# Kernel tuning notes

Measured on AMD Instinct MI355X. Metric: run time of the kernel, lower is better.

The kernel has to match this reference:

```python
import jax, jax.numpy as jnp
import numpy as np

SEQ_LEN = 32
B, H, E, HID = 2048, 512, 512, 16
BN_EPS = 1e-5

def _mlp(x, w1, b1, g, bt, m, v, w2, b2):
    # Linear -> BatchNorm1d(eval) -> ReLU -> Linear
    h = x @ w1 + b1
    h = (h - m) * jax.lax.rsqrt(v + BN_EPS) * g + bt
    h = jnp.maximum(h, 0.0)
    return h @ w2 + b2

def setup_inputs() -> dict:
    key = jax.random.key(0)
    ks = jax.random.split(key, 24)
    def rn(k, shp, s=0.05):
        return jax.random.normal(k, shp, dtype=jnp.float32) * s
    inp = {
        'last_pos': jax.random.uniform(ks[0], (B, 2), dtype=jnp.float32),
        'hh': rn(ks[1], (1, B, H), 1.0),
        'ch': rn(ks[2], (1, B, H), 1.0),
        'se_w1': rn(ks[3], (2, HID)),
        'se_b1': rn(ks[4], (HID,)),
        'se_g': jax.random.uniform(ks[5], (HID,), dtype=jnp.float32) + 0.5,
        'se_bt': rn(ks[6], (HID,)),
        'se_m': rn(ks[7], (HID,)),
        'se_v': jax.random.uniform(ks[8], (HID,), dtype=jnp.float32) + 0.5,
        'se_w2': rn(ks[9], (HID, E)),
        'se_b2': rn(ks[10], (E,)),
        'w_ih': rn(ks[11], (4 * H, E)),
        'w_hh': rn(ks[12], (4 * H, H)),
        'b_ih': rn(ks[13], (4 * H,)),
        'b_hh': rn(ks[14], (4 * H,)),
        'hp_w1': rn(ks[15], (H, HID)),
        'hp_b1': rn(ks[16], (HID,)),
        'hp_g': jax.random.uniform(ks[17], (HID,), dtype=jnp.float32) + 0.5,
        'hp_bt': rn(ks[18], (HID,)),
        'hp_m': rn(ks[19], (HID,)),
        'hp_v': jax.random.uniform(ks[20], (HID,), dtype=jnp.float32) + 0.5,
        'hp_w2': rn(ks[21], (HID, 2)),
        'hp_b2': rn(ks[22], (2,)),
    }
    return inp

def reference(last_pos, hh, ch, se_w1, se_b1, se_g, se_bt, se_m, se_v, se_w2, se_b2,
              w_ih, w_hh, b_ih, b_hh,
              hp_w1, hp_b1, hp_g, hp_bt, hp_m, hp_v, hp_w2, hp_b2):
    h0, c0 = hh[0], ch[0]  # num_layers == 1

    def step(carry, _):
        h, c, lp = carry
        x = _mlp(lp, se_w1, se_b1, se_g, se_bt, se_m, se_v, se_w2, se_b2)  # [B,E]
        gates = x @ w_ih.T + b_ih + h @ w_hh.T + b_hh                      # [B,4H]
        i, f, g, o = jnp.split(gates, 4, axis=-1)
        i = jax.nn.sigmoid(i)
        f = jax.nn.sigmoid(f)
        g = jnp.tanh(g)
        o = jax.nn.sigmoid(o)
        c = f * c + i * g
        h = o * jnp.tanh(c)
        pos_rel = _mlp(h, hp_w1, hp_b1, hp_g, hp_bt, hp_m, hp_v, hp_w2, hp_b2)  # [B,2]
        # relative_to_abs on a length-1 sequence == pos_rel + last_pos, then sigmoid
        lp = jax.nn.sigmoid(pos_rel + lp)
        return (h, c, lp), lp

    _, traj = jax.lax.scan(step, (h0, c0, last_pos), None, length=SEQ_LEN)
    return traj  # [seq_len, batch, 2]
```

## Files before the change

kernel.cpp:

```cpp
#include <hip/hip_runtime.h>


#define TSEQ  32
#define BATCH 2048
#define HDIM  512
#define GDIM  2048
#define NBLK  256
#define NTHR  512
#define DEPTH 8

typedef __bf16 bf16x8 __attribute__((ext_vector_type(8)));
typedef float  f32x16 __attribute__((ext_vector_type(16)));
typedef unsigned long long u64;

#define BS_OFF     0
#define HPW_OFF    131072
#define UNI_OFF    147456
#define H1_OFF     157696
#define LPS_OFF    161792
#define PRM_OFF    162816
#define LDS_TOTAL  163360

#define WS_W1F    0
#define WS_BIASF  131072
#define WS_FLAGS  139264
#define WS_HATOM  141312

__device__ __forceinline__ unsigned f2bf(float f) {
  unsigned u = __float_as_uint(f);
  u += 0x7fffu + ((u >> 16) & 1u);
  return u >> 16;
}
__device__ __forceinline__ float bf2f(unsigned short b) {
  return __uint_as_float(((unsigned)b) << 16);
}
__device__ __forceinline__ u64 ld8(const void* p) {
  return __hip_atomic_load((const u64*)p, __ATOMIC_RELAXED, __HIP_MEMORY_SCOPE_AGENT);
}
__device__ __forceinline__ void st8(void* p, u64 v) {
  __hip_atomic_store((u64*)p, v, __ATOMIC_RELAXED, __HIP_MEMORY_SCOPE_AGENT);
}
__device__ __forceinline__ unsigned ld4(const unsigned* p) {
  return __hip_atomic_load(p, __ATOMIC_RELAXED, __HIP_MEMORY_SCOPE_AGENT);
}
__device__ __forceinline__ void st4(unsigned* p, unsigned v) {
  __hip_atomic_store(p, v, __ATOMIC_RELAXED, __HIP_MEMORY_SCOPE_AGENT);
}
__device__ __forceinline__ void l2_inv() {
  asm volatile("buffer_inv sc1" ::: "memory");
}
#define QB(x, imm) __uint_as_float((unsigned)__builtin_amdgcn_mov_dpp((int)__float_as_uint(x), imm, 0xF, 0xF, true))

struct KParams {
  const float *last_pos, *ch0, *w_hh;
  const float *se_w1, *se_b1, *se_g, *se_bt, *se_m, *se_v;
  const float *hp_w1, *hp_b1, *hp_g, *hp_bt, *hp_m, *hp_v, *hp_w2, *hp_b2;
  const float *W1f_g, *bias_f;
  char* hatom;
  unsigned* flags;
  float* out;
};

__global__ __launch_bounds__(256) void decoder_setup(
    const float* __restrict__ w_ih, const float* __restrict__ se_w2,
    const float* __restrict__ se_b2, const float* __restrict__ b_ih,
    const float* __restrict__ b_hh, const float* __restrict__ hh,
    float* __restrict__ W1f_g, float* __restrict__ bias_f,
    char* __restrict__ hatom) {
  int bid = blockIdx.x, tid = threadIdx.x;
  if (bid < 256) {
    __shared__ float wrow[8 * 512];
    __shared__ float ps[256];
    __shared__ float psB[128];
    int r0 = bid * 8;
    #pragma unroll
    for (int i = 0; i < 4; ++i) {
      int idx = i * 256 + tid;
      ((float4*)wrow)[idx] = ((const float4*)(w_ih + (size_t)r0 * 512))[idx];
    }
    __syncthreads();
    {
      int r = tid >> 5, q = (tid >> 1) & 15, half = tid & 1;
      const float* sw = se_w2 + (size_t)q * 512 + half * 256;
      const float* wr = wrow + r * 512 + half * 256;
      float s = 0.f;
      #pragma unroll 8
      for (int e = 0; e < 256; ++e) s += sw[e] * wr[e];
      ps[tid] = s;
    }
    if (tid < 128) {
      int r = tid >> 4, seg = tid & 15;
      const float* wr = wrow + r * 512 + seg * 32;
      const float* sb = se_b2 + seg * 32;
      float s = 0.f;
      #pragma unroll
      for (int e = 0; e < 32; ++e) s += sb[e] * wr[e];
      psB[tid] = s;
    }
    __syncthreads();
    if (tid < 128) {
      int r = tid >> 4, q = tid & 15;
      W1f_g[(r0 + r) * 16 + q] = ps[r * 32 + q * 2] + ps[r * 32 + q * 2 + 1];
    } else if (tid < 136) {
      int r = tid - 128;
      float s = 0.f;
      #pragma unroll
      for (int i = 0; i < 16; ++i) s += psB[r * 16 + i];
      bias_f[r0 + r] = s + b_ih[r0 + r] + b_hh[r0 + r];
    }
  } else {
    int bb = bid - 256;
    for (int u = 0; u < 8; ++u) {
      int aidx = bb * 2048 + u * 256 + tid;
      int mtl = aidx >> 13, a = aidx & 8191;
      int lane = a & 63, slot = a >> 6;
      int m = (slot & 3) * 32 + (lane & 31);
      int k8 = (slot >> 2) * 2 + (lane >> 5);
      const float* s8 = hh + (size_t)mtl * 65536 + (size_t)m * 512 + k8 * 8;
      uint4 v;
      v.x = f2bf(s8[0]) | (f2bf(s8[1]) << 16);
      v.y = f2bf(s8[2]) | (f2bf(s8[3]) << 16);
      v.z = f2bf(s8[4]) | (f2bf(s8[5]) << 16);
      v.w = f2bf(s8[6]) | (f2bf(s8[7]) << 16);
      *(uint4*)(hatom + 2097152 + (size_t)mtl * 131072 + (size_t)a * 16) = v;
    }
  }
}

__global__ __launch_bounds__(NTHR, 2) void decoder_persist(KParams p) {
  extern __shared__ char lds[];
  const int tid  = threadIdx.x;
  const int lane = tid & 63;
  const int wid  = tid >> 6;
  const int wm   = wid >> 1;
  const int wn   = wid & 1;
  const int mt   = blockIdx.x >> 4;
  const int nt   = blockIdx.x & 15;
  const int m0   = mt * 128;

  float* prm = (float*)(lds + PRM_OFF);
  float* lps = (float*)(lds + LPS_OFF);
  float* h2s = (float*)(lds + UNI_OFF);
  unsigned short* hPsh = (unsigned short*)(lds + UNI_OFF);
  unsigned short* h1s  = (unsigned short*)(lds + H1_OFF);

  if (tid < 16) {
    int q = tid;
    float sA = p.se_g[q] * rsqrtf(p.se_v[q] + 1e-5f);
    prm[q]      = sA;
    prm[16 + q] = (p.se_b1[q] - p.se_m[q]) * sA + p.se_bt[q];
    float hA = p.hp_g[q] * rsqrtf(p.hp_v[q] + 1e-5f);
    prm[32 + q] = hA;
    prm[48 + q] = (p.hp_b1[q] - p.hp_m[q]) * hA + p.hp_bt[q];
  }
  if (tid < 32) { prm[64 + tid] = p.se_w1[tid]; prm[96 + tid] = p.hp_w2[tid]; }
  if (tid < 2)  { prm[128 + tid] = p.hp_b2[tid]; }
  if (tid < 256) lps[tid] = p.last_pos[(size_t)m0 * 2 + tid];
  float biasr[2];
  #pragma unroll
  for (int t2 = 0; t2 < 2; ++t2) {
    int n = wn * 64 + t2 * 32 + (lane & 31);
    int grow = (n & 3) * 512 + nt * 32 + (n >> 2);
    biasr[t2] = p.bias_f[grow];
  }
  for (int a = tid; a < 8192; a += NTHR) {
    int n = a >> 6, ka = a & 63;
    int grow = (n & 3) * 512 + nt * 32 + (n >> 2);
    const float* src = p.w_hh + (size_t)grow * 512 + ka * 8;
    uint4 v;
    v.x = f2bf(src[0]) | (f2bf(src[1]) << 16);
    v.y = f2bf(src[2]) | (f2bf(src[3]) << 16);
    v.z = f2bf(src[4]) | (f2bf(src[5]) << 16);
    v.w = f2bf(src[6]) | (f2bf(src[7]) << 16);
    *(uint4*)(lds + BS_OFF + ((size_t)(n * 64 + (ka ^ (n & 7)))) * 16) = v;
  }
  for (int a = tid; a < 1024; a += NTHR) {
    int n = a >> 6, k8 = a & 63;
    const float* src = p.hp_w1 + (size_t)(k8 * 8) * 16 + n;
    uint4 v;
    v.x = f2bf(src[0])   | (f2bf(src[16]) << 16);
    v.y = f2bf(src[32])  | (f2bf(src[48]) << 16);
    v.z = f2bf(src[64])  | (f2bf(src[80]) << 16);
    v.w = f2bf(src[96])  | (f2bf(src[112]) << 16);
    *(uint4*)(lds + HPW_OFF + ((size_t)(n * 64 + (k8 ^ (n & 7)))) * 16) = v;
  }
  float c_st[2][16];
  #pragma unroll
  for (int t2 = 0; t2 < 2; ++t2)
    #pragma unroll
    for (int r = 0; r < 16; ++r) c_st[t2][r] = 0.f;
  if ((lane & 3) == 0) {
    #pragma unroll
    for (int t2 = 0; t2 < 2; ++t2) {
      int n_loc = wn * 64 + t2 * 32 + (lane & 31);
      int jj = n_loc >> 2;
      #pragma unroll
      for (int r = 0; r < 16; ++r) {
        int row = (r & 3) + 8 * (r >> 2) + 4 * (lane >> 5) + wm * 32;
        c_st[t2][r] = p.ch0[(size_t)(m0 + row) * 512 + nt * 32 + jj];
      }
    }
  }
  const int n0 = wn * 64 + (lane & 31);
  const int n1 = n0 + 32;
  const int gate = lane & 3;
  const int khalf = lane >> 5;
  const int pj = ((tid >> 8) << 1) | ((tid >> 5) & 1);
  const int pm = ((tid >> 6) & 3) * 32 + (tid & 31);
  union BW { unsigned short s[8]; bf16x8 v; } w0f, w1f;
  {
    int g0 = (n0 & 3) * 512 + nt * 32 + (n0 >> 2);
    int g1 = (n1 & 3) * 512 + nt * 32 + (n1 >> 2);
    const float4* s0 = (const float4*)(p.W1f_g + (size_t)g0 * 16 + khalf * 8);
    const float4* s1 = (const float4*)(p.W1f_g + (size_t)g1 * 16 + khalf * 8);
    float4 a = s0[0], b = s0[1], c = s1[0], d = s1[1];
    w0f.s[0] = f2bf(a.x); w0f.s[1] = f2bf(a.y); w0f.s[2] = f2bf(a.z); w0f.s[3] = f2bf(a.w);
    w0f.s[4] = f2bf(b.x); w0f.s[5] = f2bf(b.y); w0f.s[6] = f2bf(b.z); w0f.s[7] = f2bf(b.w);
    w1f.s[0] = f2bf(c.x); w1f.s[1] = f2bf(c.y); w1f.s[2] = f2bf(c.z); w1f.s[3] = f2bf(c.w);
    w1f.s[4] = f2bf(d.x); w1f.s[5] = f2bf(d.y); w1f.s[6] = f2bf(d.z); w1f.s[7] = f2bf(d.w);
  }
  __syncthreads();
  float sA2q = 0.f, bA2q = 0.f;
  if ((lane & 31) < 16) { sA2q = prm[32 + (lane & 31)]; bA2q = prm[48 + (lane & 31)]; }

  for (int t = 0; t < TSEQ; ++t) {
    if (t > 0) {
      if (wid == 0) {
        const unsigned* fl = p.flags + mt * 32 + (lane & 15);
        while (!__all((int)(ld4(fl) >= (unsigned)t)))
          __builtin_amdgcn_s_sleep(2);
        l2_inv();
      }
      __syncthreads();
    }

    f32x16 acc0, acc1, accP;
    #pragma unroll
    for (int i = 0; i < 16; ++i) { acc0[i] = 0.f; acc1[i] = 0.f; accP[i] = 0.f; }
    {
      const char* abase = p.hatom + (size_t)((t + 1) & 1) * 2097152 + mt * 131072
                          + (wm * 64 + lane) * 16;
      uint4 pre[DEPTH];
      #pragma unroll
      for (int c = 0; c < DEPTH; ++c) pre[c] = *(const uint4*)(abase + c * 4096);
      union AB { uint4 u; bf16x8 v; };
      #pragma unroll
      for (int c = 0; c < 32; ++c) {
        AB u;
        u.u = pre[c & (DEPTH - 1)];
        if (c + DEPTH < 32)
          pre[c & (DEPTH - 1)] = *(const uint4*)(abase + (c + DEPTH) * 4096);
        int kal = c * 2 + khalf;
        bf16x8 b0 = *(const bf16x8*)(lds + BS_OFF + (((n0 << 6) + (kal ^ (n0 & 7))) << 4));
        bf16x8 b1 = *(const bf16x8*)(lds + BS_OFF + (((n1 << 6) + (kal ^ (n1 & 7))) << 4));
        acc0 = __builtin_amdgcn_mfma_f32_32x32x16_bf16(u.v, b0, acc0, 0, 0, 0);
        acc1 = __builtin_amdgcn_mfma_f32_32x32x16_bf16(u.v, b1, acc1, 0, 0, 0);
        if (wn == 0) {
          bf16x8 bp = {};
          if ((lane & 31) < 16)
            bp = *(const bf16x8*)(lds + HPW_OFF
                  + ((((lane & 31) << 6) + (kal ^ (lane & 7))) << 4));
          accP = __builtin_amdgcn_mfma_f32_32x32x16_bf16(u.v, bp, accP, 0, 0, 0);
        }
      }
    }

    if (t > 0) {
      if (wn == 0 && (lane & 31) < 16) {
        int q = lane & 31;
        #pragma unroll
        for (int r = 0; r < 16; ++r) {
          int row = (r & 3) + 8 * (r >> 2) + 4 * (lane >> 5) + wm * 32;
          h2s[row * 20 + q] = fmaxf(accP[r] * sA2q + bA2q, 0.f);
        }
      }
      __syncthreads();
      if (tid < 256) {
        int m = tid >> 1, c = tid & 1;
        float a2 = prm[128 + c];
        const float4* hrow = (const float4*)(lds + UNI_OFF + m * 80);
        #pragma unroll
        for (int g4 = 0; g4 < 4; ++g4) {
          float4 v = hrow[g4];
          a2 += v.x * prm[96 + (g4 * 4 + 0) * 2 + c];
          a2 += v.y * prm[96 + (g4 * 4 + 1) * 2 + c];
          a2 += v.z * prm[96 + (g4 * 4 + 2) * 2 + c];
          a2 += v.w * prm[96 + (g4 * 4 + 3) * 2 + c];
        }
        float lpv = 1.f / (1.f + __expf(-(a2 + lps[tid])));
        lps[tid] = lpv;
        if (nt == 0)
          st4((unsigned*)&p.out[((size_t)(t - 1) * BATCH + m0 + m) * 2 + c],
              __float_as_uint(lpv));
      }
      __syncthreads();
    }

    #pragma unroll
    for (int u = 0; u < 4; ++u) {
      int id = u * NTHR + tid;
      int m = id >> 4, q = id & 15;
      float z = lps[m * 2] * prm[64 + q] + lps[m * 2 + 1] * prm[80 + q];
      h1s[m * 16 + q] = (unsigned short)f2bf(fmaxf(z * prm[q] + prm[16 + q], 0.f));
    }
    __syncthreads();

    {
      bf16x8 a1 = *(const bf16x8*)(lds + H1_OFF + (wm * 32 + (lane & 31)) * 32 + khalf * 16);
      acc0 = __builtin_amdgcn_mfma_f32_32x32x16_bf16(a1, w0f.v, acc0, 0, 0, 0);
      acc1 = __builtin_amdgcn_mfma_f32_32x32x16_bf16(a1, w1f.v, acc1, 0, 0, 0);
    }

    #pragma unroll
    for (int t2 = 0; t2 < 2; ++t2) {
      float bias = biasr[t2];
      int jj = (wn * 64 + t2 * 32 + (lane & 31)) >> 2;
      float act[16];
      const f32x16& A = (t2 == 0) ? acc0 : acc1;
      #pragma unroll
      for (int r = 0; r < 16; ++r) {
        float v = A[r] + bias;
        float vv = (gate == 2) ? 2.f * v : v;
        float sg = 1.f / (1.f + __expf(-vv));
        act[r] = (gate == 2) ? 2.f * sg - 1.f : sg;
      }
      #pragma unroll
      for (int r = 0; r < 16; ++r) {
        float iv = QB(act[r], 0x00);
        float fv = QB(act[r], 0x55);
        float gv = QB(act[r], 0xAA);
        float ov = QB(act[r], 0xFF);
        float cn = fv * c_st[t2][r] + iv * gv;
        c_st[t2][r] = cn;
        float th = 2.f / (1.f + __expf(-2.f * cn)) - 1.f;
        float hn = ov * th;
        if ((lane & 3) == 0) {
          int row = (r & 3) + 8 * (r >> 2) + 4 * (lane >> 5) + wm * 32;
          hPsh[row * 36 + jj] = (unsigned short)f2bf(hn);
        }
      }
    }
    __syncthreads();

    {
      const u64* hp8 = (const u64*)(lds + UNI_OFF + pm * 72 + pj * 16);
      u64* hdst = (u64*)(p.hatom + (size_t)(t & 1) * 2097152 + mt * 131072);
      st8(hdst + (512 * nt + tid) * 2,     hp8[0]);
      st8(hdst + (512 * nt + tid) * 2 + 1, hp8[1]);
    }
    __syncthreads();
    if (tid == 0) st4(p.flags + mt * 32 + nt, (unsigned)(t + 1));
  }

  {
    if (wid == 0) {
      const unsigned* fl = p.flags + mt * 32 + (lane & 15);
      while (!__all((int)(ld4(fl) >= (unsigned)TSEQ)))
        __builtin_amdgcn_s_sleep(2);
      l2_inv();
    }
    __syncthreads();
    f32x16 accP;
    #pragma unroll
    for (int i = 0; i < 16; ++i) accP[i] = 0.f;
    if (wn == 0) {
      const char* abase = p.hatom + 2097152 + mt * 131072 + (wm * 64 + lane) * 16;
      uint4 pre[DEPTH];
      #pragma unroll
      for (int c = 0; c < DEPTH; ++c) pre[c] = *(const uint4*)(abase + c * 4096);
      union AB { uint4 u; bf16x8 v; };
      #pragma unroll
      for (int c = 0; c < 32; ++c) {
        AB u;
        u.u = pre[c & (DEPTH - 1)];
        if (c + DEPTH < 32)
          pre[c & (DEPTH - 1)] = *(const uint4*)(abase + (c + DEPTH) * 4096);
        int kal = c * 2 + khalf;
        bf16x8 bp = {};
        if ((lane & 31) < 16)
          bp = *(const bf16x8*)(lds + HPW_OFF
                + ((((lane & 31) << 6) + (kal ^ (lane & 7))) << 4));
        accP = __builtin_amdgcn_mfma_f32_32x32x16_bf16(u.v, bp, accP, 0, 0, 0);
      }
      if ((lane & 31) < 16) {
        int q = lane & 31;
        #pragma unroll
        for (int r = 0; r < 16; ++r) {
          int row = (r & 3) + 8 * (r >> 2) + 4 * (lane >> 5) + wm * 32;
          h2s[row * 20 + q] = fmaxf(accP[r] * sA2q + bA2q, 0.f);
        }
      }
    }
    __syncthreads();
    if (tid < 256 && nt == 0) {
      int m = tid >> 1, c = tid & 1;
      float a2 = prm[128 + c];
      const float4* hrow = (const float4*)(lds + UNI_OFF + m * 80);
      #pragma unroll
      for (int g4 = 0; g4 < 4; ++g4) {
        float4 v = hrow[g4];
        a2 += v.x * prm[96 + (g4 * 4 + 0) * 2 + c];
        a2 += v.y * prm[96 + (g4 * 4 + 1) * 2 + c];
        a2 += v.z * prm[96 + (g4 * 4 + 2) * 2 + c];
        a2 += v.w * prm[96 + (g4 * 4 + 3) * 2 + c];
      }
      float lpv = 1.f / (1.f + __expf(-(a2 + lps[tid])));
      st4((unsigned*)&p.out[((size_t)(TSEQ - 1) * BATCH + m0 + m) * 2 + c],
          __float_as_uint(lpv));
    }
  }
}

extern "C" void kernel_launch(void* const* d_in, const int* in_sizes, int n_in,
                              void* d_out, int out_size, void* d_ws, size_t ws_size,
                              hipStream_t stream) {
  char* ws = (char*)d_ws;
  const float* last_pos = (const float*)d_in[0];
  const float* hh    = (const float*)d_in[1];
  const float* ch    = (const float*)d_in[2];
  const float* se_w1 = (const float*)d_in[3];
  const float* se_b1 = (const float*)d_in[4];
  const float* se_g  = (const float*)d_in[5];
  const float* se_bt = (const float*)d_in[6];
  const float* se_m  = (const float*)d_in[7];
  const float* se_v  = (const float*)d_in[8];
  const float* se_w2 = (const float*)d_in[9];
  const float* se_b2 = (const float*)d_in[10];
  const float* w_ih  = (const float*)d_in[11];
  const float* w_hh  = (const float*)d_in[12];
  const float* b_ih  = (const float*)d_in[13];
  const float* b_hh  = (const float*)d_in[14];
  const float* hp_w1 = (const float*)d_in[15];
  const float* hp_b1 = (const float*)d_in[16];
  const float* hp_g  = (const float*)d_in[17];
  const float* hp_bt = (const float*)d_in[18];
  const float* hp_m  = (const float*)d_in[19];
  const float* hp_v  = (const float*)d_in[20];
  const float* hp_w2 = (const float*)d_in[21];
  const float* hp_b2 = (const float*)d_in[22];

  float* W1f_g  = (float*)(ws + WS_W1F);
  float* bias_f = (float*)(ws + WS_BIASF);
  unsigned* flags = (unsigned*)(ws + WS_FLAGS);
  char* hatom   = ws + WS_HATOM;

  (void)hipMemsetAsync(ws + WS_FLAGS, 0, 2048, stream);
  decoder_setup<<<dim3(320), dim3(256), 0, stream>>>(
      w_ih, se_w2, se_b2, b_ih, b_hh, hh, W1f_g, bias_f, hatom);

  (void)hipFuncSetAttribute((const void*)decoder_persist,
                            hipFuncAttributeMaxDynamicSharedMemorySize, LDS_TOTAL);

  KParams kp;
  kp.last_pos = last_pos; kp.ch0 = ch; kp.w_hh = w_hh;
  kp.se_w1 = se_w1; kp.se_b1 = se_b1; kp.se_g = se_g; kp.se_bt = se_bt;
  kp.se_m = se_m; kp.se_v = se_v;
  kp.hp_w1 = hp_w1; kp.hp_b1 = hp_b1; kp.hp_g = hp_g; kp.hp_bt = hp_bt;
  kp.hp_m = hp_m; kp.hp_v = hp_v; kp.hp_w2 = hp_w2; kp.hp_b2 = hp_b2;
  kp.W1f_g = W1f_g; kp.bias_f = bias_f;
  kp.hatom = hatom; kp.flags = flags; kp.out = (float*)d_out;

  void* args[] = { &kp };
  (void)hipLaunchCooperativeKernel((void*)decoder_persist, dim3(NBLK), dim3(NTHR),
                                   args, LDS_TOTAL, stream);
}
```

Measured before the change: 615.9 us.

## Replace per-step block barrier with per-producer fine-grained readiness polling

Instead of waiting for all 16 producer blocks' flags before a step, each wave polls the flags with a ballot and starts loading K-chunks from whichever producer is ready, rotating its start chunk by its own tile index. The L2 invalidate moves to the producer side before publishing the flag, and the cooperative launch is replaced by a normal launch. This aims to overlap the recurrent matmul with straggling producers and cut barrier latency. The invalidate placement is unusual, so consumers may read stale lines, and a normal launch no longer guarantees all blocks are co-resident.

```diff
diff --git a/kernel.cpp b/kernel.cpp
--- a/kernel.cpp
+++ b/kernel.cpp
@@ -33,9 +33,6 @@
 }
 __device__ __forceinline__ float bf2f(unsigned short b) {
   return __uint_as_float(((unsigned)b) << 16);
-}
-__device__ __forceinline__ u64 ld8(const void* p) {
-  return __hip_atomic_load((const u64*)p, __ATOMIC_RELAXED, __HIP_MEMORY_SCOPE_AGENT);
 }
 __device__ __forceinline__ void st8(void* p, u64 v) {
   __hip_atomic_store((u64*)p, v, __ATOMIC_RELAXED, __HIP_MEMORY_SCOPE_AGENT);
@@ -220,36 +217,48 @@
     w1f.s[4] = f2bf(d.x); w1f.s[5] = f2bf(d.y); w1f.s[6] = f2bf(d.z); w1f.s[7] = f2bf(d.w);
   }
   __syncthreads();
+  if (tid == 0) l2_inv();
+  __syncthreads();
   float sA2q = 0.f, bA2q = 0.f;
   if ((lane & 31) < 16) { sA2q = prm[32 + (lane & 31)]; bA2q = prm[48 + (lane & 31)]; }
 
+  const unsigned* fl = p.flags + mt * 32 + (lane & 15);
+
   for (int t = 0; t < TSEQ; ++t) {
-    if (t > 0) {
-      if (wid == 0) {
-        const unsigned* fl = p.flags + mt * 32 + (lane & 15);
-        while (!__all((int)(ld4(fl) >= (unsigned)t)))
-          __builtin_amdgcn_s_sleep(2);
-        l2_inv();
-      }
-      __syncthreads();
-    }
-
     f32x16 acc0, acc1, accP;
     #pragma unroll
     for (int i = 0; i < 16; ++i) { acc0[i] = 0.f; acc1[i] = 0.f; accP[i] = 0.f; }
     {
       const char* abase = p.hatom + (size_t)((t + 1) & 1) * 2097152 + mt * 131072
                           + (wm * 64 + lane) * 16;
+      const unsigned tgt = (unsigned)t;
+      u64 rdy = (t == 0) ? 0xffffull : (1ull << nt);
       uint4 pre[DEPTH];
       #pragma unroll
-      for (int c = 0; c < DEPTH; ++c) pre[c] = *(const uint4*)(abase + c * 4096);
+      for (int j = 0; j < DEPTH; ++j) {
+        int src = (nt + (j >> 1)) & 15;
+        while (!((rdy >> src) & 1)) {
+          rdy = __ballot(ld4(fl) >= tgt);
+          __builtin_amdgcn_s_sleep(1);
+        }
+        pre[j] = *(const uint4*)(abase + ((src << 1) | (j & 1)) * 4096);
+      }
       union AB { uint4 u; bf16x8 v; };
       #pragma unroll
-      for (int c = 0; c < 32; ++c) {
+      for (int j = 0; j < 32; ++j) {
+        int c = (((nt + (j >> 1)) & 15) << 1) | (j & 1);
         AB u;
-        u.u = pre[c & (DEPTH - 1)];
-        if (c + DEPTH < 32)
-          pre[c & (DEPTH - 1)] = *(const uint4*)(abase + (c + DEPTH) * 4096);
+        u.u = pre[j & (DEPTH - 1)];
+        int jn = j + DEPTH;
+        if (jn < 32) {
+          int srcn = (nt + (jn >> 1)) & 15;
+          while (!((rdy >> srcn) & 1)) {
+            rdy = __ballot(ld4(fl) >= tgt);
+            __builtin_amdgcn_s_sleep(1);
+          }
+          pre[j & (DEPTH - 1)] =
+              *(const uint4*)(abase + ((srcn << 1) | (jn & 1)) * 4096);
+        }
         int kal = c * 2 + khalf;
         bf16x8 b0 = *(const bf16x8*)(lds + BS_OFF + (((n0 << 6) + (kal ^ (n0 & 7))) << 4));
         bf16x8 b1 = *(const bf16x8*)(lds + BS_OFF + (((n1 << 6) + (kal ^ (n1 & 7))) << 4));
@@ -349,15 +358,16 @@
       st8(hdst + (512 * nt + tid) * 2 + 1, hp8[1]);
     }
     __syncthreads();
-    if (tid == 0) st4(p.flags + mt * 32 + nt, (unsigned)(t + 1));
+    if (wid == 0) {
+      l2_inv();
+      if (lane == 0) st4(p.flags + mt * 32 + nt, (unsigned)(t + 1));
+    }
   }
 
   {
     if (wid == 0) {
-      const unsigned* fl = p.flags + mt * 32 + (lane & 15);
-      while (!__all((int)(ld4(fl) >= (unsigned)TSEQ)))
+      while (__ballot(ld4(fl) >= (unsigned)TSEQ) != ~0ull)
         __builtin_amdgcn_s_sleep(2);
-      l2_inv();
     }
     __syncthreads();
     f32x16 accP;
@@ -460,7 +470,5 @@
   kp.W1f_g = W1f_g; kp.bias_f = bias_f;
   kp.hatom = hatom; kp.flags = flags; kp.out = (float*)d_out;
 
-  void* args[] = { &kp };
-  (void)hipLaunchCooperativeKernel((void*)decoder_persist, dim3(NBLK), dim3(NTHR),
-                                   args, LDS_TOTAL, stream);
-}
+  decoder_persist<<<dim3(NBLK), dim3(NTHR), LDS_TOTAL, stream>>>(kp);
+}
```

New measurement: 587.1 us. 1.05x faster.

## Fold setup kernel into persistent kernel and fuse pos-MLP into step epilogue

Applied to the files above, without the earlier changes.

Removes the separate setup launch. Each block now computes its own slice of the fused W_ih·se_w2 weight and bias with MFMA and writes its bf16 h0 slice, with flags signalling readiness. The per-step lp sigmoid and the input-MLP h1 computation are merged into one pass with a DPP swap, which drops a barrier. The cooperative launch becomes a normal launch. In exchange each block redoes some weight folding, the folded weight now goes through bf16 MFMA, and grid co-residency is no longer guaranteed by the runtime.

```diff
diff --git a/kernel.cpp b/kernel.cpp
--- a/kernel.cpp
+++ b/kernel.cpp
@@ -4,7 +4,6 @@
 #define TSEQ  32
 #define BATCH 2048
 #define HDIM  512
-#define GDIM  2048
 #define NBLK  256
 #define NTHR  512
 #define DEPTH 8
@@ -20,23 +19,17 @@
 #define LPS_OFF    161792
 #define PRM_OFF    162816
 #define LDS_TOTAL  163360
-
-#define WS_W1F    0
-#define WS_BIASF  131072
-#define WS_FLAGS  139264
-#define WS_HATOM  141312
+#define W1T_OFF    32768
+#define BT_OFF     41472
+
+#define WS_FLAGS  0
+#define WS_HATOM  2048
 
 __device__ __forceinline__ unsigned f2bf(float f) {
   unsigned u = __float_as_uint(f);
   u += 0x7fffu + ((u >> 16) & 1u);
   return u >> 16;
 }
-__device__ __forceinline__ float bf2f(unsigned short b) {
-  return __uint_as_float(((unsigned)b) << 16);
-}
-__device__ __forceinline__ u64 ld8(const void* p) {
-  return __hip_atomic_load((const u64*)p, __ATOMIC_RELAXED, __HIP_MEMORY_SCOPE_AGENT);
-}
 __device__ __forceinline__ void st8(void* p, u64 v) {
   __hip_atomic_store((u64*)p, v, __ATOMIC_RELAXED, __HIP_MEMORY_SCOPE_AGENT);
 }
@@ -52,80 +45,13 @@
 #define QB(x, imm) __uint_as_float((unsigned)__builtin_amdgcn_mov_dpp((int)__float_as_uint(x), imm, 0xF, 0xF, true))
 
 struct KParams {
-  const float *last_pos, *ch0, *w_hh;
-  const float *se_w1, *se_b1, *se_g, *se_bt, *se_m, *se_v;
+  const float *last_pos, *hh, *ch0, *w_hh, *w_ih, *b_ih, *b_hh;
+  const float *se_w1, *se_b1, *se_g, *se_bt, *se_m, *se_v, *se_w2, *se_b2;
   const float *hp_w1, *hp_b1, *hp_g, *hp_bt, *hp_m, *hp_v, *hp_w2, *hp_b2;
-  const float *W1f_g, *bias_f;
   char* hatom;
   unsigned* flags;
   float* out;
 };
-
-__global__ __launch_bounds__(256) void decoder_setup(
-    const float* __restrict__ w_ih, const float* __restrict__ se_w2,
-    const float* __restrict__ se_b2, const float* __restrict__ b_ih,
-    const float* __restrict__ b_hh, const float* __restrict__ hh,
-    float* __restrict__ W1f_g, float* __restrict__ bias_f,
-    char* __restrict__ hatom) {
-  int bid = blockIdx.x, tid = threadIdx.x;
-  if (bid < 256) {
-    __shared__ float wrow[8 * 512];
-    __shared__ float ps[256];
-    __shared__ float psB[128];
-    int r0 = bid * 8;
-    #pragma unroll
-    for (int i = 0; i < 4; ++i) {
-      int idx = i * 256 + tid;
-      ((float4*)wrow)[idx] = ((const float4*)(w_ih + (size_t)r0 * 512))[idx];
-    }
-    __syncthreads();
-    {
-      int r = tid >> 5, q = (tid >> 1) & 15, half = tid & 1;
-      const float* sw = se_w2 + (size_t)q * 512 + half * 256;
-      const float* wr = wrow + r * 512 + half * 256;
-      float s = 0.f;
-      #pragma unroll 8
-      for (int e = 0; e < 256; ++e) s += sw[e] * wr[e];
-      ps[tid] = s;
-    }
-    if (tid < 128) {
-      int r = tid >> 4, seg = tid & 15;
-      const float* wr = wrow + r * 512 + seg * 32;
-      const float* sb = se_b2 + seg * 32;
-      float s = 0.f;
-      #pragma unroll
-      for (int e = 0; e < 32; ++e) s += sb[e] * wr[e];
-      psB[tid] = s;
-    }
-    __syncthreads();
-    if (tid < 128) {
-      int r = tid >> 4, q = tid & 15;
-      W1f_g[(r0 + r) * 16 + q] = ps[r * 32 + q * 2] + ps[r * 32 + q * 2 + 1];
-    } else if (tid < 136) {
-      int r = tid - 128;
-      float s = 0.f;
-      #pragma unroll
-      for (int i = 0; i < 16; ++i) s += psB[r * 16 + i];
-      bias_f[r0 + r] = s + b_ih[r0 + r] + b_hh[r0 + r];
-    }
-  } else {
-    int bb = bid - 256;
-    for (int u = 0; u < 8; ++u) {
-      int aidx = bb * 2048 + u * 256 + tid;
-      int mtl = aidx >> 13, a = aidx & 8191;
-      int lane = a & 63, slot = a >> 6;
-      int m = (slot & 3) * 32 + (lane & 31);
-      int k8 = (slot >> 2) * 2 + (lane >> 5);
-      const float* s8 = hh + (size_t)mtl * 65536 + (size_t)m * 512 + k8 * 8;
-      uint4 v;
-      v.x = f2bf(s8[0]) | (f2bf(s8[1]) << 16);
-      v.y = f2bf(s8[2]) | (f2bf(s8[3]) << 16);
-      v.z = f2bf(s8[4]) | (f2bf(s8[5]) << 16);
-      v.w = f2bf(s8[6]) | (f2bf(s8[7]) << 16);
-      *(uint4*)(hatom + 2097152 + (size_t)mtl * 131072 + (size_t)a * 16) = v;
-    }
-  }
-}
 
 __global__ __launch_bounds__(NTHR, 2) void decoder_persist(KParams p) {
   extern __shared__ char lds[];
@@ -142,7 +68,15 @@
   float* lps = (float*)(lds + LPS_OFF);
   float* h2s = (float*)(lds + UNI_OFF);
   unsigned short* hPsh = (unsigned short*)(lds + UNI_OFF);
-  unsigned short* h1s  = (unsigned short*)(lds + H1_OFF);
+  float* W1T = (float*)(lds + W1T_OFF);
+  float* bT  = (float*)(lds + BT_OFF);
+
+  const int n0 = wn * 64 + (lane & 31);
+  const int n1 = n0 + 32;
+  const int gate = lane & 3;
+  const int khalf = lane >> 5;
+  const int pj = ((tid >> 8) << 1) | ((tid >> 5) & 1);
+  const int pm = ((tid >> 6) & 3) * 32 + (tid & 31);
 
   if (tid < 16) {
     int q = tid;
@@ -156,13 +90,90 @@
   if (tid < 32) { prm[64 + tid] = p.se_w1[tid]; prm[96 + tid] = p.hp_w2[tid]; }
   if (tid < 2)  { prm[128 + tid] = p.hp_b2[tid]; }
   if (tid < 256) lps[tid] = p.last_pos[(size_t)m0 * 2 + tid];
+
+  for (int a = tid; a < 2048; a += NTHR) {
+    int n = a >> 6, k8 = a & 63;
+    uint4 v = {0, 0, 0, 0};
+    if (n <= 16) {
+      const float* src = (n < 16) ? (p.se_w2 + (size_t)n * 512 + k8 * 8)
+                                  : (p.se_b2 + k8 * 8);
+      v.x = f2bf(src[0]) | (f2bf(src[1]) << 16);
+      v.y = f2bf(src[2]) | (f2bf(src[3]) << 16);
+      v.z = f2bf(src[4]) | (f2bf(src[5]) << 16);
+      v.w = f2bf(src[6]) | (f2bf(src[7]) << 16);
+    }
+    *(uint4*)(lds + BS_OFF + ((size_t)(n * 64 + (k8 ^ (n & 7)))) * 16) = v;
+  }
+  __syncthreads();
+
+  if ((wid & 1) == 0) {
+    int rloc = wm * 32 + (lane & 31);
+    int grow = (rloc & 3) * 512 + nt * 32 + (rloc >> 2);
+    const float* arow = p.w_ih + (size_t)grow * 512;
+    f32x16 accW;
+    #pragma unroll
+    for (int i = 0; i < 16; ++i) accW[i] = 0.f;
+    float4 pa[4], pb[4];
+    #pragma unroll
+    for (int j = 0; j < 4; ++j) {
+      int kal = j * 2 + khalf;
+      pa[j] = ((const float4*)(arow + kal * 8))[0];
+      pb[j] = ((const float4*)(arow + kal * 8))[1];
+    }
+    #pragma unroll
+    for (int c = 0; c < 32; ++c) {
+      int kal = c * 2 + khalf;
+      union { unsigned short s[8]; bf16x8 v; } av;
+      float4 a = pa[c & 3], b = pb[c & 3];
+      av.s[0] = f2bf(a.x); av.s[1] = f2bf(a.y); av.s[2] = f2bf(a.z); av.s[3] = f2bf(a.w);
+      av.s[4] = f2bf(b.x); av.s[5] = f2bf(b.y); av.s[6] = f2bf(b.z); av.s[7] = f2bf(b.w);
+      if (c + 4 < 32) {
+        int kn = (c + 4) * 2 + khalf;
+        pa[c & 3] = ((const float4*)(arow + kn * 8))[0];
+        pb[c & 3] = ((const float4*)(arow + kn * 8))[1];
+      }
+      int q = lane & 31;
+      bf16x8 bp = *(const bf16x8*)(lds + BS_OFF + (((q << 6) + (kal ^ (q & 7))) << 4));
+      accW = __builtin_amdgcn_mfma_f32_32x32x16_bf16(av.v, bp, accW, 0, 0, 0);
+    }
+    int q = lane & 31;
+    #pragma unroll
+    for (int r = 0; r < 16; ++r) {
+      int row = (r & 3) + 8 * (r >> 2) + 4 * khalf + wm * 32;
+      if (q < 16) {
+        W1T[row * 17 + q] = accW[r];
+      } else if (q == 16) {
+        int g2 = (row & 3) * 512 + nt * 32 + (row >> 2);
+        bT[row] = accW[r] + p.b_ih[g2] + p.b_hh[g2];
+      }
+    }
+  }
+  __syncthreads();
+
+  union BW { unsigned short s[8]; bf16x8 v; } w0f, w1f;
+  #pragma unroll
+  for (int j = 0; j < 8; ++j) {
+    w0f.s[j] = (unsigned short)f2bf(W1T[n0 * 17 + khalf * 8 + j]);
+    w1f.s[j] = (unsigned short)f2bf(W1T[n1 * 17 + khalf * 8 + j]);
+  }
   float biasr[2];
-  #pragma unroll
-  for (int t2 = 0; t2 < 2; ++t2) {
-    int n = wn * 64 + t2 * 32 + (lane & 31);
-    int grow = (n & 3) * 512 + nt * 32 + (n >> 2);
-    biasr[t2] = p.bias_f[grow];
-  }
+  biasr[0] = bT[wn * 64 + (lane & 31)];
+  biasr[1] = bT[wn * 64 + 32 + (lane & 31)];
+  {
+    const float* src = p.hh + (size_t)(m0 + pm) * 512 + nt * 32 + pj * 8;
+    float4 f0 = ((const float4*)src)[0];
+    float4 f1 = ((const float4*)src)[1];
+    u64 lo = (u64)f2bf(f0.x) | ((u64)f2bf(f0.y) << 16)
+           | ((u64)f2bf(f0.z) << 32) | ((u64)f2bf(f0.w) << 48);
+    u64 hi = (u64)f2bf(f1.x) | ((u64)f2bf(f1.y) << 16)
+           | ((u64)f2bf(f1.z) << 32) | ((u64)f2bf(f1.w) << 48);
+    u64* hdst = (u64*)(p.hatom + 2097152 + mt * 131072);
+    st8(hdst + (512 * nt + tid) * 2,     lo);
+    st8(hdst + (512 * nt + tid) * 2 + 1, hi);
+  }
+  __syncthreads();
+  if (tid == 0) st4(p.flags + mt * 32 + nt, 1u);
+
   for (int a = tid; a < 8192; a += NTHR) {
     int n = a >> 6, ka = a & 63;
     int grow = (n & 3) * 512 + nt * 32 + (n >> 2);
@@ -178,10 +189,10 @@
     int n = a >> 6, k8 = a & 63;
     const float* src = p.hp_w1 + (size_t)(k8 * 8) * 16 + n;
     uint4 v;
-    v.x = f2bf(src[0])   | (f2bf(src[16]) << 16);
-    v.y = f2bf(src[32])  | (f2bf(src[48]) << 16);
-    v.z = f2bf(src[64])  | (f2bf(src[80]) << 16);
-    v.w = f2bf(src[96])  | (f2bf(src[112]) << 16);
+    v.x = f2bf(src[0])  | (f2bf(src[16]) << 16);
+    v.y = f2bf(src[32]) | (f2bf(src[48]) << 16);
+    v.z = f2bf(src[64]) | (f2bf(src[80]) << 16);
+    v.w = f2bf(src[96]) | (f2bf(src[112]) << 16);
     *(uint4*)(lds + HPW_OFF + ((size_t)(n * 64 + (k8 ^ (n & 7)))) * 16) = v;
   }
   float c_st[2][16];
@@ -192,47 +203,27 @@
   if ((lane & 3) == 0) {
     #pragma unroll
     for (int t2 = 0; t2 < 2; ++t2) {
-      int n_loc = wn * 64 + t2 * 32 + (lane & 31);
-      int jj = n_loc >> 2;
+      int jj = (wn * 64 + t2 * 32 + (lane & 31)) >> 2;
       #pragma unroll
       for (int r = 0; r < 16; ++r) {
-        int row = (r & 3) + 8 * (r >> 2) + 4 * (lane >> 5) + wm * 32;
+        int row = (r & 3) + 8 * (r >> 2) + 4 * khalf + wm * 32;
         c_st[t2][r] = p.ch0[(size_t)(m0 + row) * 512 + nt * 32 + jj];
       }
     }
   }
-  const int n0 = wn * 64 + (lane & 31);
-  const int n1 = n0 + 32;
-  const int gate = lane & 3;
-  const int khalf = lane >> 5;
-  const int pj = ((tid >> 8) << 1) | ((tid >> 5) & 1);
-  const int pm = ((tid >> 6) & 3) * 32 + (tid & 31);
-  union BW { unsigned short s[8]; bf16x8 v; } w0f, w1f;
-  {
-    int g0 = (n0 & 3) * 512 + nt * 32 + (n0 >> 2);
-    int g1 = (n1 & 3) * 512 + nt * 32 + (n1 >> 2);
-    const float4* s0 = (const float4*)(p.W1f_g + (size_t)g0 * 16 + khalf * 8);
-    const float4* s1 = (const float4*)(p.W1f_g + (size_t)g1 * 16 + khalf * 8);
-    float4 a = s0[0], b = s0[1], c = s1[0], d = s1[1];
-    w0f.s[0] = f2bf(a.x); w0f.s[1] = f2bf(a.y); w0f.s[2] = f2bf(a.z); w0f.s[3] = f2bf(a.w);
-    w0f.s[4] = f2bf(b.x); w0f.s[5] = f2bf(b.y); w0f.s[6] = f2bf(b.z); w0f.s[7] = f2bf(b.w);
-    w1f.s[0] = f2bf(c.x); w1f.s[1] = f2bf(c.y); w1f.s[2] = f2bf(c.z); w1f.s[3] = f2bf(c.w);
-    w1f.s[4] = f2bf(d.x); w1f.s[5] = f2bf(d.y); w1f.s[6] = f2bf(d.z); w1f.s[7] = f2bf(d.w);
-  }
   __syncthreads();
+
   float sA2q = 0.f, bA2q = 0.f;
   if ((lane & 31) < 16) { sA2q = prm[32 + (lane & 31)]; bA2q = prm[48 + (lane & 31)]; }
+  const unsigned* fl = p.flags + mt * 32 + (lane & 15);
 
   for (int t = 0; t < TSEQ; ++t) {
-    if (t > 0) {
-      if (wid == 0) {
-        const unsigned* fl = p.flags + mt * 32 + (lane & 15);
-        while (!__all((int)(ld4(fl) >= (unsigned)t)))
-          __builtin_amdgcn_s_sleep(2);
-        l2_inv();
-      }
-      __syncthreads();
-    }
+    if (wid == 0) {
+      while (!__all((int)(ld4(fl) >= (unsigned)(t + 1))))
+        __builtin_amdgcn_s_sleep(2);
+      l2_inv();
+    }
+    __syncthreads();
 
     f32x16 acc0, acc1, accP;
     #pragma unroll
@@ -270,13 +261,17 @@
         int q = lane & 31;
         #pragma unroll
         for (int r = 0; r < 16; ++r) {
-          int row = (r & 3) + 8 * (r >> 2) + 4 * (lane >> 5) + wm * 32;
+          int row = (r & 3) + 8 * (r >> 2) + 4 * khalf + wm * 32;
           h2s[row * 20 + q] = fmaxf(accP[r] * sA2q + bA2q, 0.f);
         }
       }
       __syncthreads();
-      if (tid < 256) {
-        int m = tid >> 1, c = tid & 1;
+    }
+
+    if (tid < 256) {
+      int m = tid >> 1, c = tid & 1;
+      float lp0, lp1;
+      if (t > 0) {
         float a2 = prm[128 + c];
         const float4* hrow = (const float4*)(lds + UNI_OFF + m * 80);
         #pragma unroll
@@ -292,16 +287,28 @@
         if (nt == 0)
           st4((unsigned*)&p.out[((size_t)(t - 1) * BATCH + m0 + m) * 2 + c],
               __float_as_uint(lpv));
-      }
-      __syncthreads();
-    }
-
-    #pragma unroll
-    for (int u = 0; u < 4; ++u) {
-      int id = u * NTHR + tid;
-      int m = id >> 4, q = id & 15;
-      float z = lps[m * 2] * prm[64 + q] + lps[m * 2 + 1] * prm[80 + q];
-      h1s[m * 16 + q] = (unsigned short)f2bf(fmaxf(z * prm[q] + prm[16 + q], 0.f));
+        float other = QB(lpv, 0xB1);
+        lp0 = c ? other : lpv;
+        lp1 = c ? lpv : other;
+      } else {
+        lp0 = lps[m * 2];
+        lp1 = lps[m * 2 + 1];
+      }
+      u64 hq[2];
+      #pragma unroll
+      for (int half = 0; half < 2; ++half) {
+        u64 w = 0;
+        #pragma unroll
+        for (int i = 0; i < 4; ++i) {
+          int q = c * 8 + half * 4 + i;
+          float z = lp0 * prm[64 + q] + lp1 * prm[80 + q];
+          w |= (u64)f2bf(fmaxf(z * prm[q] + prm[16 + q], 0.f)) << (16 * i);
+        }
+        hq[half] = w;
+      }
+      u64* hd = (u64*)(lds + H1_OFF + m * 32 + c * 16);
+      hd[0] = hq[0];
+      hd[1] = hq[1];
     }
     __syncthreads();
 
@@ -335,7 +342,7 @@
         float th = 2.f / (1.f + __expf(-2.f * cn)) - 1.f;
         float hn = ov * th;
         if ((lane & 3) == 0) {
-          int row = (r & 3) + 8 * (r >> 2) + 4 * (lane >> 5) + wm * 32;
+          int row = (r & 3) + 8 * (r >> 2) + 4 * khalf + wm * 32;
           hPsh[row * 36 + jj] = (unsigned short)f2bf(hn);
         }
       }
@@ -349,13 +356,12 @@
       st8(hdst + (512 * nt + tid) * 2 + 1, hp8[1]);
     }
     __syncthreads();
-    if (tid == 0) st4(p.flags + mt * 32 + nt, (unsigned)(t + 1));
+    if (tid == 0) st4(p.flags + mt * 32 + nt, (unsigned)(t + 2));
   }
 
   {
     if (wid == 0) {
-      const unsigned* fl = p.flags + mt * 32 + (lane & 15);
-      while (!__all((int)(ld4(fl) >= (unsigned)TSEQ)))
+      while (!__all((int)(ld4(fl) >= (unsigned)(TSEQ + 1))))
         __builtin_amdgcn_s_sleep(2);
       l2_inv();
     }
@@ -386,7 +392,7 @@
         int q = lane & 31;
         #pragma unroll
         for (int r = 0; r < 16; ++r) {
-          int row = (r & 3) + 8 * (r >> 2) + 4 * (lane >> 5) + wm * 32;
+          int row = (r & 3) + 8 * (r >> 2) + 4 * khalf + wm * 32;
           h2s[row * 20 + q] = fmaxf(accP[r] * sA2q + bA2q, 0.f);
         }
       }
@@ -415,52 +421,36 @@
                               void* d_out, int out_size, void* d_ws, size_t ws_size,
                               hipStream_t stream) {
   char* ws = (char*)d_ws;
-  const float* last_pos = (const float*)d_in[0];
-  const float* hh    = (const float*)d_in[1];
-  const float* ch    = (const float*)d_in[2];
-  const float* se_w1 = (const float*)d_in[3];
-  const float* se_b1 = (const float*)d_in[4];
-  const float* se_g  = (const float*)d_in[5];
-  const float* se_bt = (const float*)d_in[6];
-  const float* se_m  = (const float*)d_in[7];
-  const float* se_v  = (const float*)d_in[8];
-  const float* se_w2 = (const float*)d_in[9];
-  const float* se_b2 = (const float*)d_in[10];
-  const float* w_ih  = (const float*)d_in[11];
-  const float* w_hh  = (const float*)d_in[12];
-  const float* b_ih  = (const float*)d_in[13];
-  const float* b_hh  = (const float*)d_in[14];
-  const float* hp_w1 = (const float*)d_in[15];
-  const float* hp_b1 = (const float*)d_in[16];
-  const float* hp_g  = (const float*)d_in[17];
-  const float* hp_bt = (const float*)d_in[18];
-  const float* hp_m  = (const float*)d_in[19];
-  const float* hp_v  = (const float*)d_in[20];
-  const float* hp_w2 = (const float*)d_in[21];
-  const float* hp_b2 = (const float*)d_in[22];
-
-  float* W1f_g  = (float*)(ws + WS_W1F);
-  float* bias_f = (float*)(ws + WS_BIASF);
-  unsigned* flags = (unsigned*)(ws + WS_FLAGS);
-  char* hatom   = ws + WS_HATOM;
+  KParams kp;
+  kp.last_pos = (const float*)d_in[0];
+  kp.hh    = (const float*)d_in[1];
+  kp.ch0   = (const float*)d_in[2];
+  kp.se_w1 = (const float*)d_in[3];
+  kp.se_b1 = (const float*)d_in[4];
+  kp.se_g  = (const float*)d_in[5];
+  kp.se_bt = (const float*)d_in[6];
+  kp.se_m  = (const float*)d_in[7];
+  kp.se_v  = (const float*)d_in[8];
+  kp.se_w2 = (const float*)d_in[9];
+  kp.se_b2 = (const float*)d_in[10];
+  kp.w_ih  = (const float*)d_in[11];
+  kp.w_hh  = (const float*)d_in[12];
+  kp.b_ih  = (const float*)d_in[13];
+  kp.b_hh  = (const float*)d_in[14];
+  kp.hp_w1 = (const float*)d_in[15];
+  kp.hp_b1 = (const float*)d_in[16];
+  kp.hp_g  = (const float*)d_in[17];
+  kp.hp_bt = (const float*)d_in[18];
+  kp.hp_m  = (const float*)d_in[19];
+  kp.hp_v  = (const float*)d_in[20];
+  kp.hp_w2 = (const float*)d_in[21];
+  kp.hp_b2 = (const float*)d_in[22];
+  kp.flags = (unsigned*)(ws + WS_FLAGS);
+  kp.hatom = ws + WS_HATOM;
+  kp.out   = (float*)d_out;
 
   (void)hipMemsetAsync(ws + WS_FLAGS, 0, 2048, stream);
-  decoder_setup<<<dim3(320), dim3(256), 0, stream>>>(
-      w_ih, se_w2, se_b2, b_ih, b_hh, hh, W1f_g, bias_f, hatom);
-
   (void)hipFuncSetAttribute((const void*)decoder_persist,
                             hipFuncAttributeMaxDynamicSharedMemorySize, LDS_TOTAL);
-
-  KParams kp;
-  kp.last_pos = last_pos; kp.ch0 = ch; kp.w_hh = w_hh;
-  kp.se_w1 = se_w1; kp.se_b1 = se_b1; kp.se_g = se_g; kp.se_bt = se_bt;
-  kp.se_m = se_m; kp.se_v = se_v;
-  kp.hp_w1 = hp_w1; kp.hp_b1 = hp_b1; kp.hp_g = hp_g; kp.hp_bt = hp_bt;
-  kp.hp_m = hp_m; kp.hp_v = hp_v; kp.hp_w2 = hp_w2; kp.hp_b2 = hp_b2;
-  kp.W1f_g = W1f_g; kp.bias_f = bias_f;
-  kp.hatom = hatom; kp.flags = flags; kp.out = (float*)d_out;
-
-  void* args[] = { &kp };
-  (void)hipLaunchCooperativeKernel((void*)decoder_persist, dim3(NBLK), dim3(NTHR),
-                                   args, LDS_TOTAL, stream);
-}
+  decoder_persist<<<dim3(NBLK), dim3(NTHR), LDS_TOTAL, stream>>>(kp);
+}
```

Measured after the change: 526.6 us. 14.5% less time.
